# Optimization experiments

Hardware: AMD Instinct MI355X
Metric: run time of the kernel (lower is better)

The kernel has to match this reference:

```python
import jax, jax.numpy as jnp
import numpy as np
import math

HIDDEN = 1024
ADAPTER = 256

def gelu_new(x):
    # BERT/GPT tanh-approx gelu, matches the torch code exactly
    return 0.5 * x * (1.0 + jnp.tanh(math.sqrt(2.0 / math.pi) * (x + 0.044715 * x ** 3)))

def setup_inputs() -> dict:
    key = jax.random.key(0)
    k1, k2, k3 = jax.random.split(key, 3)
    hidden_states = jax.random.normal(k1, (8, 4096, HIDDEN), dtype=jnp.float32)
    # LayerNorm params: weight=1, bias=0 per init_bert_weights
    ln_weight = jnp.ones((HIDDEN,), jnp.float32)
    ln_bias = jnp.zeros((HIDDEN,), jnp.float32)
    # Linear weights ~ N(0, 0.02), biases zero
    w_down = jax.random.normal(k2, (HIDDEN, ADAPTER), jnp.float32) * 0.02
    b_down = jnp.zeros((ADAPTER,), jnp.float32)
    w_up = jax.random.normal(k3, (ADAPTER, HIDDEN), jnp.float32) * 0.02
    b_up = jnp.zeros((HIDDEN,), jnp.float32)
    return {"hidden_states": hidden_states, "ln_weight": ln_weight, "ln_bias": ln_bias,
            "w_down": w_down, "b_down": b_down, "w_up": w_up, "b_up": b_up}

def layer_norm(x, weight, bias, eps=1e-5):
    mean = jnp.mean(x, axis=-1, keepdims=True)
    var = jnp.mean(jnp.square(x - mean), axis=-1, keepdims=True)
    return (x - mean) * jax.lax.rsqrt(var + eps) * weight + bias

def reference(hidden_states, ln_weight, ln_bias, w_down, b_down, w_up, b_up):
    h = layer_norm(hidden_states, ln_weight, ln_bias)           # [B,S,H]
    h = gelu_new(jnp.einsum('bsh,ha->bsa', h, w_down) + b_down)  # [B,S,A]
    h = jnp.einsum('bsa,ah->bsh', h, w_up) + b_up                # [B,S,H]
    return h + hidden_states
```

## Files before the change

kernel.cpp:

```cpp
#include <hip/hip_runtime.h>
#include <hip/hip_bf16.h>

#define HID 1024
#define ADP 256
#define MB  32

typedef short s16x8 __attribute__((ext_vector_type(8)));
typedef float f32x4 __attribute__((ext_vector_type(4)));

__device__ __forceinline__ unsigned short f2bf(float f) {
    union { float f; unsigned int u; } v; v.f = f;
    unsigned int r = v.u + 0x7fffu + ((v.u >> 16) & 1u);
    return (unsigned short)(r >> 16);
}

__device__ __forceinline__ float gelu_new_f(float x) {
    float t = 0.7978845608028654f * x * (1.0f + 0.044715f * x * x);
    t = fminf(fmaxf(t, -15.f), 15.f);
    float e = __expf(-2.0f * t);
    float th = (1.0f - e) / (1.0f + e);
    return 0.5f * x * (1.0f + th);
}

__global__ void transpose_cvt(const float* __restrict__ in, unsigned short* __restrict__ out,
                              int R, int C) {
    __shared__ float t[32][33];
    int r0 = blockIdx.y * 32, c0 = blockIdx.x * 32;
    int tx = threadIdx.x, ty = threadIdx.y;
    #pragma unroll
    for (int j = 0; j < 32; j += 8)
        t[ty + j][tx] = in[(size_t)(r0 + ty + j) * C + c0 + tx];
    __syncthreads();
    #pragma unroll
    for (int j = 0; j < 32; j += 8)
        out[(size_t)(c0 + ty + j) * R + r0 + tx] = f2bf(t[tx][ty + j]);
}

__global__ void prep_uv(const float* __restrict__ wd, const float* __restrict__ lnw,
                        const float* __restrict__ lnb, float* __restrict__ U,
                        float* __restrict__ V) {
    int a = threadIdx.x;
    int h0 = blockIdx.x * 64;
    float pu = 0.f, pv = 0.f;
    #pragma unroll 8
    for (int i = 0; i < 64; ++i) {
        float w = wd[(size_t)(h0 + i) * ADP + a];
        pu += lnw[h0 + i] * w;
        pv += lnb[h0 + i] * w;
    }
    atomicAdd(&U[a], pu);
    atomicAdd(&V[a], pv);
}

__global__ __launch_bounds__(256, 4)
void adapter_fused(const float* __restrict__ x,
                   const float* __restrict__ lnw,
                   const float* __restrict__ U, const float* __restrict__ V,
                   const float* __restrict__ bdn, const float* __restrict__ bup,
                   const unsigned short* __restrict__ WdT,
                   const unsigned short* __restrict__ WuT,
                   float* __restrict__ out)
{
    __shared__ unsigned short a_h[32][264];
    __shared__ float ep[4][16][66];
    __shared__ float U_s[256];
    __shared__ float W2_s[256];
    __shared__ float stats[32][2];

    const int tid  = threadIdx.x;
    const int wv   = tid >> 6;
    const int lane = tid & 63;
    const int q    = lane >> 4;
    const int l15  = lane & 15;
    const long row0 = (long)blockIdx.x * MB;

    U_s[tid]  = U[tid];
    W2_s[tid] = V[tid] + bdn[tid];

    const int r   = tid >> 3;
    const int sub = tid & 7;

    f32x4 c1[2][4];
    #pragma unroll
    for (int a = 0; a < 2; ++a)
        #pragma unroll
        for (int b = 0; b < 4; ++b)
            c1[a][b] = (f32x4){0.f, 0.f, 0.f, 0.f};

    float s = 0.f, ss = 0.f;

    for (int kc = 0; kc < 4; ++kc) {
        {
            const float4* xr = (const float4*)(x + (row0 + r) * HID + kc * 256);
            const float4* wr = (const float4*)(lnw + kc * 256);
            #pragma unroll
            for (int i = 0; i < 8; ++i) {
                int f4 = sub + 8 * i;
                float4 v = xr[f4], w4 = wr[f4];
                s  += v.x + v.y + v.z + v.w;
                ss += v.x * v.x + v.y * v.y + v.z * v.z + v.w * v.w;
                ushort4 o;
                o.x = f2bf(v.x * w4.x); o.y = f2bf(v.y * w4.y);
                o.z = f2bf(v.z * w4.z); o.w = f2bf(v.w * w4.w);
                *(ushort4*)&a_h[r][f4 * 4] = o;
            }
        }
        __syncthreads();
        const int nb = wv * 64;
        #pragma unroll
        for (int ks = 0; ks < 8; ++ks) {
            int kof = ks * 32 + q * 8;
            s16x8 af[2], bfr[4];
            #pragma unroll
            for (int mt = 0; mt < 2; ++mt)
                af[mt] = *(const s16x8*)&a_h[mt * 16 + l15][kof];
            #pragma unroll
            for (int nt = 0; nt < 4; ++nt)
                bfr[nt] = *(const s16x8*)&WdT[(size_t)(nb + nt * 16 + l15) * HID + kc * 256 + kof];
            #pragma unroll
            for (int mt = 0; mt < 2; ++mt)
                #pragma unroll
                for (int nt = 0; nt < 4; ++nt)
                    c1[mt][nt] = __builtin_amdgcn_mfma_f32_16x16x32_bf16(af[mt], bfr[nt], c1[mt][nt], 0, 0, 0);
        }
        __syncthreads();
    }

    s += __shfl_xor(s, 1); ss += __shfl_xor(ss, 1);
    s += __shfl_xor(s, 2); ss += __shfl_xor(ss, 2);
    s += __shfl_xor(s, 4); ss += __shfl_xor(ss, 4);
    if (sub == 0) {
        float mean = s * (1.f / HID);
        float var  = ss * (1.f / HID) - mean * mean;
        stats[r][0] = mean;
        stats[r][1] = rsqrtf(var + 1e-5f);
    }
    __syncthreads();

    #pragma unroll
    for (int mt = 0; mt < 2; ++mt)
        #pragma unroll
        for (int nt = 0; nt < 4; ++nt) {
            int n = wv * 64 + nt * 16 + l15;
            float u = U_s[n], w2 = W2_s[n];
            #pragma unroll
            for (int rr = 0; rr < 4; ++rr) {
                int m = mt * 16 + q * 4 + rr;
                float mean = stats[m][0], rstd = stats[m][1];
                float val = rstd * c1[mt][nt][rr] - rstd * mean * u + w2;
                a_h[m][n] = f2bf(gelu_new_f(val));
            }
        }
    __syncthreads();

    for (int ncc = 0; ncc < 4; ++ncc) {
        const int cb = wv * 256 + ncc * 64;
        f32x4 c2[2][4];
        #pragma unroll
        for (int a = 0; a < 2; ++a)
            #pragma unroll
            for (int b = 0; b < 4; ++b)
                c2[a][b] = (f32x4){0.f, 0.f, 0.f, 0.f};
        #pragma unroll
        for (int ks = 0; ks < 8; ++ks) {
            int kof = ks * 32 + q * 8;
            s16x8 af[2], bfr[4];
            #pragma unroll
            for (int mt = 0; mt < 2; ++mt)
                af[mt] = *(const s16x8*)&a_h[mt * 16 + l15][kof];
            #pragma unroll
            for (int nt = 0; nt < 4; ++nt)
                bfr[nt] = *(const s16x8*)&WuT[(size_t)(cb + nt * 16 + l15) * ADP + kof];
            #pragma unroll
            for (int mt = 0; mt < 2; ++mt)
                #pragma unroll
                for (int nt = 0; nt < 4; ++nt)
                    c2[mt][nt] = __builtin_amdgcn_mfma_f32_16x16x32_bf16(af[mt], bfr[nt], c2[mt][nt], 0, 0, 0);
        }
        #pragma unroll
        for (int mt = 0; mt < 2; ++mt) {
            #pragma unroll
            for (int nt = 0; nt < 4; ++nt)
                #pragma unroll
                for (int rr = 0; rr < 4; ++rr)
                    ep[wv][q * 4 + rr][nt * 16 + l15] = c2[mt][nt][rr];
            __builtin_amdgcn_s_waitcnt(0xc07f);
            int er = lane >> 2, c4 = lane & 3;
            long gm = row0 + mt * 16 + er;
            const float4* xr = (const float4*)(x + gm * HID + cb);
            const float4* br = (const float4*)(bup + cb);
            float4* orow     = (float4*)(out + gm * HID + cb);
            #pragma unroll
            for (int i = 0; i < 4; ++i) {
                int f4 = i * 4 + c4;
                float4 v  = *(const float4*)&ep[wv][er][f4 * 4];
                float4 rs = xr[f4];
                float4 bu = br[f4];
                v.x += rs.x + bu.x; v.y += rs.y + bu.y;
                v.z += rs.z + bu.z; v.w += rs.w + bu.w;
                orow[f4] = v;
            }
            __builtin_amdgcn_s_waitcnt(0xc07f);
        }
    }
}

extern "C" void kernel_launch(void* const* d_in, const int* in_sizes, int n_in,
                              void* d_out, int out_size, void* d_ws, size_t ws_size,
                              hipStream_t stream) {
    const float* x   = (const float*)d_in[0];
    const float* lnw = (const float*)d_in[1];
    const float* lnb = (const float*)d_in[2];
    const float* wd  = (const float*)d_in[3];
    const float* bd  = (const float*)d_in[4];
    const float* wu  = (const float*)d_in[5];
    const float* bu  = (const float*)d_in[6];
    float* out = (float*)d_out;

    unsigned short* WdT = (unsigned short*)d_ws;
    unsigned short* WuT = WdT + (size_t)HID * ADP;
    float* U = (float*)(WuT + (size_t)HID * ADP);
    float* V = U + ADP;

    hipMemsetAsync(U, 0, 2 * ADP * sizeof(float), stream);
    prep_uv<<<HID / 64, ADP, 0, stream>>>(wd, lnw, lnb, U, V);

    transpose_cvt<<<dim3(ADP / 32, HID / 32), dim3(32, 8), 0, stream>>>(wd, WdT, HID, ADP);
    transpose_cvt<<<dim3(HID / 32, ADP / 32), dim3(32, 8), 0, stream>>>(wu, WuT, ADP, HID);

    const int rows = in_sizes[0] / HID;
    adapter_fused<<<rows / MB, 256, 0, stream>>>(x, lnw, U, V, bd, bu, WdT, WuT, out);
}
```

Measured before the change: 403.1 us.

## Split fused adapter into down and up kernels with bf16 intermediate

Measured after the change: 441.0 us. 9.4% more time.

```diff
diff --git a/kernel.cpp b/kernel.cpp
--- a/kernel.cpp
+++ b/kernel.cpp
@@ -3,10 +3,10 @@
 
 #define HID 1024
 #define ADP 256
-#define MB  32
 
 typedef short s16x8 __attribute__((ext_vector_type(8)));
 typedef float f32x4 __attribute__((ext_vector_type(4)));
+typedef unsigned short us16x16 __attribute__((ext_vector_type(16)));
 
 __device__ __forceinline__ unsigned short f2bf(float f) {
     union { float f; unsigned int u; } v; v.f = f;
@@ -52,33 +52,26 @@
     atomicAdd(&V[a], pv);
 }
 
-__global__ __launch_bounds__(256, 4)
-void adapter_fused(const float* __restrict__ x,
-                   const float* __restrict__ lnw,
-                   const float* __restrict__ U, const float* __restrict__ V,
-                   const float* __restrict__ bdn, const float* __restrict__ bup,
-                   const unsigned short* __restrict__ WdT,
-                   const unsigned short* __restrict__ WuT,
-                   float* __restrict__ out)
+__global__ __launch_bounds__(256, 2)
+void adapter_down(const float* __restrict__ x, const float* __restrict__ lnw,
+                  const float* __restrict__ U, const float* __restrict__ V,
+                  const float* __restrict__ bdn,
+                  const unsigned short* __restrict__ WdT,
+                  unsigned short* __restrict__ h)
 {
-    __shared__ unsigned short a_h[32][264];
-    __shared__ float ep[4][16][66];
-    __shared__ float U_s[256];
-    __shared__ float W2_s[256];
-    __shared__ float stats[32][2];
-
-    const int tid  = threadIdx.x;
-    const int wv   = tid >> 6;
-    const int lane = tid & 63;
-    const int q    = lane >> 4;
-    const int l15  = lane & 15;
-    const long row0 = (long)blockIdx.x * MB;
-
-    U_s[tid]  = U[tid];
-    W2_s[tid] = V[tid] + bdn[tid];
-
-    const int r   = tid >> 3;
-    const int sub = tid & 7;
+    __shared__ unsigned short ep[4][16][72];
+    const int tid = threadIdx.x, wv = tid >> 6, lane = tid & 63;
+    const int q = lane >> 4, l15 = lane & 15;
+    const long row0 = (long)blockIdx.x * 32;
+    const int nb = wv * 64;
+
+    float u4[4], w24[4];
+    #pragma unroll
+    for (int nt = 0; nt < 4; ++nt) {
+        int n = nb + nt * 16 + l15;
+        u4[nt]  = U[n];
+        w24[nt] = V[n] + bdn[n];
+    }
 
     f32x4 c1[2][4];
     #pragma unroll
@@ -86,96 +79,108 @@
         #pragma unroll
         for (int b = 0; b < 4; ++b)
             c1[a][b] = (f32x4){0.f, 0.f, 0.f, 0.f};
-
-    float s = 0.f, ss = 0.f;
-
-    for (int kc = 0; kc < 4; ++kc) {
-        {
-            const float4* xr = (const float4*)(x + (row0 + r) * HID + kc * 256);
-            const float4* wr = (const float4*)(lnw + kc * 256);
-            #pragma unroll
-            for (int i = 0; i < 8; ++i) {
-                int f4 = sub + 8 * i;
-                float4 v = xr[f4], w4 = wr[f4];
-                s  += v.x + v.y + v.z + v.w;
-                ss += v.x * v.x + v.y * v.y + v.z * v.z + v.w * v.w;
-                ushort4 o;
-                o.x = f2bf(v.x * w4.x); o.y = f2bf(v.y * w4.y);
-                o.z = f2bf(v.z * w4.z); o.w = f2bf(v.w * w4.w);
-                *(ushort4*)&a_h[r][f4 * 4] = o;
+    float s0 = 0.f, ss0 = 0.f, s1 = 0.f, ss1 = 0.f;
+
+    for (int ks = 0; ks < 32; ++ks) {
+        const int k0 = ks * 32 + q * 8;
+        float4 w0 = *(const float4*)(lnw + k0);
+        float4 w1 = *(const float4*)(lnw + k0 + 4);
+        s16x8 af[2];
+        #pragma unroll
+        for (int mt = 0; mt < 2; ++mt) {
+            const float* px = x + (row0 + mt * 16 + l15) * HID + k0;
+            float4 a0 = *(const float4*)px;
+            float4 a1 = *(const float4*)(px + 4);
+            float ps  = a0.x + a0.y + a0.z + a0.w + a1.x + a1.y + a1.z + a1.w;
+            float pss = a0.x*a0.x + a0.y*a0.y + a0.z*a0.z + a0.w*a0.w
+                      + a1.x*a1.x + a1.y*a1.y + a1.z*a1.z + a1.w*a1.w;
+            if (mt == 0) { s0 += ps; ss0 += pss; } else { s1 += ps; ss1 += pss; }
+            unsigned short o[8];
+            o[0]=f2bf(a0.x*w0.x); o[1]=f2bf(a0.y*w0.y); o[2]=f2bf(a0.z*w0.z); o[3]=f2bf(a0.w*w0.w);
+            o[4]=f2bf(a1.x*w1.x); o[5]=f2bf(a1.y*w1.y); o[6]=f2bf(a1.z*w1.z); o[7]=f2bf(a1.w*w1.w);
+            af[mt] = *(const s16x8*)o;
+        }
+        s16x8 bfr[4];
+        #pragma unroll
+        for (int nt = 0; nt < 4; ++nt)
+            bfr[nt] = *(const s16x8*)&WdT[(size_t)(nb + nt * 16 + l15) * HID + k0];
+        #pragma unroll
+        for (int mt = 0; mt < 2; ++mt)
+            #pragma unroll
+            for (int nt = 0; nt < 4; ++nt)
+                c1[mt][nt] = __builtin_amdgcn_mfma_f32_16x16x32_bf16(af[mt], bfr[nt], c1[mt][nt], 0, 0, 0);
+    }
+
+    s0 += __shfl_xor(s0, 16); ss0 += __shfl_xor(ss0, 16);
+    s0 += __shfl_xor(s0, 32); ss0 += __shfl_xor(ss0, 32);
+    s1 += __shfl_xor(s1, 16); ss1 += __shfl_xor(ss1, 16);
+    s1 += __shfl_xor(s1, 32); ss1 += __shfl_xor(ss1, 32);
+    float rstd[2], rmu[2];
+    {
+        float m0 = s0 * (1.f / HID), m1 = s1 * (1.f / HID);
+        float v0 = ss0 * (1.f / HID) - m0 * m0, v1 = ss1 * (1.f / HID) - m1 * m1;
+        rstd[0] = rsqrtf(v0 + 1e-5f); rstd[1] = rsqrtf(v1 + 1e-5f);
+        rmu[0] = rstd[0] * m0;        rmu[1] = rstd[1] * m1;
+    }
+
+    #pragma unroll
+    for (int mt = 0; mt < 2; ++mt) {
+        #pragma unroll
+        for (int rr = 0; rr < 4; ++rr) {
+            int srcl = q * 4 + rr;
+            float rs = __shfl(rstd[mt], srcl);
+            float rm = __shfl(rmu[mt],  srcl);
+            #pragma unroll
+            for (int nt = 0; nt < 4; ++nt) {
+                float val = rs * c1[mt][nt][rr] - rm * u4[nt] + w24[nt];
+                ep[wv][q * 4 + rr][nt * 16 + l15] = f2bf(gelu_new_f(val));
             }
         }
-        __syncthreads();
-        const int nb = wv * 64;
+        __builtin_amdgcn_s_waitcnt(0xc07f);
+        int er = lane >> 2, c4 = lane & 3;
+        us16x16 vv = *(const us16x16*)&ep[wv][er][c4 * 16];
+        *(us16x16*)&h[(row0 + mt * 16 + er) * ADP + nb + c4 * 16] = vv;
+        __builtin_amdgcn_s_waitcnt(0xc07f);
+    }
+}
+
+__global__ __launch_bounds__(256, 2)
+void adapter_up(const unsigned short* __restrict__ h,
+                const unsigned short* __restrict__ WuT,
+                const float* __restrict__ x, const float* __restrict__ bup,
+                float* __restrict__ out)
+{
+    __shared__ float ep[4][16][68];
+    const int tid = threadIdx.x, wv = tid >> 6, lane = tid & 63;
+    const int q = lane >> 4, l15 = lane & 15;
+    const long row0 = (long)blockIdx.x * 32;
+
+    s16x8 af[2][8];
+    #pragma unroll
+    for (int mt = 0; mt < 2; ++mt)
+        #pragma unroll
+        for (int ks = 0; ks < 8; ++ks)
+            af[mt][ks] = *(const s16x8*)&h[(row0 + mt * 16 + l15) * ADP + ks * 32 + q * 8];
+
+    for (int ncc = 0; ncc < 4; ++ncc) {
+        const int cb = wv * 256 + ncc * 64;
+        f32x4 c2[2][4];
+        #pragma unroll
+        for (int a = 0; a < 2; ++a)
+            #pragma unroll
+            for (int b = 0; b < 4; ++b)
+                c2[a][b] = (f32x4){0.f, 0.f, 0.f, 0.f};
         #pragma unroll
         for (int ks = 0; ks < 8; ++ks) {
-            int kof = ks * 32 + q * 8;
-            s16x8 af[2], bfr[4];
-            #pragma unroll
-            for (int mt = 0; mt < 2; ++mt)
-                af[mt] = *(const s16x8*)&a_h[mt * 16 + l15][kof];
+            s16x8 bfr[4];
             #pragma unroll
             for (int nt = 0; nt < 4; ++nt)
-                bfr[nt] = *(const s16x8*)&WdT[(size_t)(nb + nt * 16 + l15) * HID + kc * 256 + kof];
+                bfr[nt] = *(const s16x8*)&WuT[(size_t)(cb + nt * 16 + l15) * ADP + ks * 32 + q * 8];
             #pragma unroll
             for (int mt = 0; mt < 2; ++mt)
                 #pragma unroll
                 for (int nt = 0; nt < 4; ++nt)
-                    c1[mt][nt] = __builtin_amdgcn_mfma_f32_16x16x32_bf16(af[mt], bfr[nt], c1[mt][nt], 0, 0, 0);
-        }
-        __syncthreads();
-    }
-
-    s += __shfl_xor(s, 1); ss += __shfl_xor(ss, 1);
-    s += __shfl_xor(s, 2); ss += __shfl_xor(ss, 2);
-    s += __shfl_xor(s, 4); ss += __shfl_xor(ss, 4);
-    if (sub == 0) {
-        float mean = s * (1.f / HID);
-        float var  = ss * (1.f / HID) - mean * mean;
-        stats[r][0] = mean;
-        stats[r][1] = rsqrtf(var + 1e-5f);
-    }
-    __syncthreads();
-
-    #pragma unroll
-    for (int mt = 0; mt < 2; ++mt)
-        #pragma unroll
-        for (int nt = 0; nt < 4; ++nt) {
-            int n = wv * 64 + nt * 16 + l15;
-            float u = U_s[n], w2 = W2_s[n];
-            #pragma unroll
-            for (int rr = 0; rr < 4; ++rr) {
-                int m = mt * 16 + q * 4 + rr;
-                float mean = stats[m][0], rstd = stats[m][1];
-                float val = rstd * c1[mt][nt][rr] - rstd * mean * u + w2;
-                a_h[m][n] = f2bf(gelu_new_f(val));
-            }
-        }
-    __syncthreads();
-
-    for (int ncc = 0; ncc < 4; ++ncc) {
-        const int cb = wv * 256 + ncc * 64;
-        f32x4 c2[2][4];
-        #pragma unroll
-        for (int a = 0; a < 2; ++a)
-            #pragma unroll
-            for (int b = 0; b < 4; ++b)
-                c2[a][b] = (f32x4){0.f, 0.f, 0.f, 0.f};
-        #pragma unroll
-        for (int ks = 0; ks < 8; ++ks) {
-            int kof = ks * 32 + q * 8;
-            s16x8 af[2], bfr[4];
-            #pragma unroll
-            for (int mt = 0; mt < 2; ++mt)
-                af[mt] = *(const s16x8*)&a_h[mt * 16 + l15][kof];
-            #pragma unroll
-            for (int nt = 0; nt < 4; ++nt)
-                bfr[nt] = *(const s16x8*)&WuT[(size_t)(cb + nt * 16 + l15) * ADP + kof];
-            #pragma unroll
-            for (int mt = 0; mt < 2; ++mt)
-                #pragma unroll
-                for (int nt = 0; nt < 4; ++nt)
-                    c2[mt][nt] = __builtin_amdgcn_mfma_f32_16x16x32_bf16(af[mt], bfr[nt], c2[mt][nt], 0, 0, 0);
+                    c2[mt][nt] = __builtin_amdgcn_mfma_f32_16x16x32_bf16(af[mt][ks], bfr[nt], c2[mt][nt], 0, 0, 0);
         }
         #pragma unroll
         for (int mt = 0; mt < 2; ++mt) {
@@ -187,18 +192,17 @@
             __builtin_amdgcn_s_waitcnt(0xc07f);
             int er = lane >> 2, c4 = lane & 3;
             long gm = row0 + mt * 16 + er;
-            const float4* xr = (const float4*)(x + gm * HID + cb);
-            const float4* br = (const float4*)(bup + cb);
-            float4* orow     = (float4*)(out + gm * HID + cb);
+            const float* xr = x + gm * HID + cb + c4 * 16;
+            const float* br = bup + cb + c4 * 16;
+            float* po       = out + gm * HID + cb + c4 * 16;
             #pragma unroll
             for (int i = 0; i < 4; ++i) {
-                int f4 = i * 4 + c4;
-                float4 v  = *(const float4*)&ep[wv][er][f4 * 4];
-                float4 rs = xr[f4];
-                float4 bu = br[f4];
+                float4 v  = *(const float4*)&ep[wv][er][c4 * 16 + i * 4];
+                float4 rs = *(const float4*)(xr + i * 4);
+                float4 bu = *(const float4*)(br + i * 4);
                 v.x += rs.x + bu.x; v.y += rs.y + bu.y;
                 v.z += rs.z + bu.z; v.w += rs.w + bu.w;
-                orow[f4] = v;
+                *(float4*)(po + i * 4) = v;
             }
             __builtin_amdgcn_s_waitcnt(0xc07f);
         }
@@ -217,17 +221,19 @@
     const float* bu  = (const float*)d_in[6];
     float* out = (float*)d_out;
 
+    const int rows = in_sizes[0] / HID;
+
     unsigned short* WdT = (unsigned short*)d_ws;
     unsigned short* WuT = WdT + (size_t)HID * ADP;
     float* U = (float*)(WuT + (size_t)HID * ADP);
     float* V = U + ADP;
+    unsigned short* h = (unsigned short*)(V + ADP);
 
     hipMemsetAsync(U, 0, 2 * ADP * sizeof(float), stream);
     prep_uv<<<HID / 64, ADP, 0, stream>>>(wd, lnw, lnb, U, V);
-
     transpose_cvt<<<dim3(ADP / 32, HID / 32), dim3(32, 8), 0, stream>>>(wd, WdT, HID, ADP);
     transpose_cvt<<<dim3(HID / 32, ADP / 32), dim3(32, 8), 0, stream>>>(wu, WuT, ADP, HID);
 
-    const int rows = in_sizes[0] / HID;
-    adapter_fused<<<rows / MB, 256, 0, stream>>>(x, lnw, U, V, bd, bu, WdT, WuT, out);
-}
+    adapter_down<<<rows / 32, 256, 0, stream>>>(x, lnw, U, V, bd, WdT, h);
+    adapter_up<<<rows / 32, 256, 0, stream>>>(h, WuT, x, bu, out);
+}
```
